# Optimization experiments

Hardware: AMD Instinct MI355X
Metric: run time of the kernel (lower is better)

The kernel has to match this reference:

```python
import jax, jax.numpy as jnp
import numpy as np


def setup_inputs() -> dict:
    key = jax.random.key(0)
    k1, k2, k3, k4 = jax.random.split(key, 4)
    B, A, C = 16, 65536, 21  # batch, anchors, num_classes+1 (20 fg classes + background)
    loc_preds = jax.random.normal(k1, (B, A, 4), dtype=jnp.float32)
    loc_targets = jax.random.normal(k2, (B, A, 4), dtype=jnp.float32)
    cls_preds = jax.random.normal(k3, (B, A, C), dtype=jnp.float32)
    # -1 = ignore, 0 = background/negative, 1..20 = positive classes
    cls_targets = jax.random.randint(k4, (B, A), -1, C)
    pos = cls_targets > 0
    return {
        "loc_preds": loc_preds,
        "loc_targets": loc_targets,
        "cls_preds": cls_preds,
        "cls_targets": cls_targets,
        "pos": pos,
        "verbose": 0,
    }


def reference(loc_preds, loc_targets, cls_preds, cls_targets, pos, verbose):
    eps = 1e-7
    num_pos = jnp.sum(pos).astype(loc_preds.dtype)

    # smooth L1 over positive anchors (sum reduction, beta=1), mask instead of gather
    posf = pos[..., None].astype(loc_preds.dtype)          # [B, A, 1]
    d = loc_preds - loc_targets
    ad = jnp.abs(d)
    sl1 = jnp.where(ad < 1.0, 0.5 * d * d, ad - 0.5)
    loc_loss = jnp.sum(sl1 * posf)

    # focal loss over non-ignored anchors (cls_targets > -1)
    pos_neg = (cls_targets > -1)[..., None].astype(cls_preds.dtype)  # [B, A, 1]
    C = cls_preds.shape[-1]
    y = jax.nn.one_hot(cls_targets, C, dtype=cls_preds.dtype)  # -1 -> all zeros
    p = jax.nn.softmax(cls_preds, axis=-1)
    p = jnp.clip(p, eps, 1.0 - eps)
    fl = -y * jnp.log(p) * (1.0 - p) ** 2
    cls_loss = jnp.sum(fl * pos_neg)

    return (loc_loss + cls_loss) / num_pos
```

## Files before the change

### kernel.cpp

```cpp
#include <hip/hip_runtime.h>

#define NCLS 21
#define BLK 256
#define CHUNK 256
#define STAGE_BYTES (CHUNK * NCLS * 4)

__device__ __forceinline__ void load_lds16(const void* g, void* l) {
    __builtin_amdgcn_global_load_lds(
        (const __attribute__((address_space(1))) unsigned int*)g,
        (__attribute__((address_space(3))) unsigned int*)l,
        16, 0, 0);
}

__global__ __launch_bounds__(BLK) void focal_main(
    const float* __restrict__ loc_p,
    const float* __restrict__ loc_t,
    const float* __restrict__ cls_p,
    const int*   __restrict__ cls_t,
    float2* __restrict__ partials,
    int n_anchors)
{
    __shared__ float lds[CHUNK * NCLS];
    __shared__ float red[8];

    const int tid  = threadIdx.x;
    const int wave = tid >> 6;
    const int lane = tid & 63;
    const long long anchor0 = (long long)blockIdx.x * CHUNK;
    const long long a = anchor0 + tid;

    if (anchor0 + CHUNK <= n_anchors) {
        const char* gbase = (const char*)(cls_p + anchor0 * NCLS);
        char* lbase = (char*)lds;
        #pragma unroll
        for (int k = wave; k < NCLS; k += 4) {
            load_lds16(gbase + k * 1024 + lane * 16, lbase + k * 1024);
        }
    } else {
        long long rem = n_anchors - anchor0;
        int valid = rem > 0 ? (int)(rem * NCLS) : 0;
        for (int i = tid; i < valid; i += BLK)
            lds[i] = cls_p[anchor0 * NCLS + i];
    }

    int t = -1;
    float4 lp = make_float4(0.f, 0.f, 0.f, 0.f);
    float4 lt = make_float4(0.f, 0.f, 0.f, 0.f);
    if (a < n_anchors) {
        t  = cls_t[a];
        lp = ((const float4*)loc_p)[a];
        lt = ((const float4*)loc_t)[a];
    }

    float acc  = 0.0f;
    float npos = 0.0f;
    {
        float d0 = lp.x - lt.x, d1 = lp.y - lt.y, d2 = lp.z - lt.z, d3 = lp.w - lt.w;
        float a0 = fabsf(d0), a1 = fabsf(d1), a2 = fabsf(d2), a3 = fabsf(d3);
        float s = 0.0f;
        s += (a0 < 1.0f) ? 0.5f * d0 * d0 : a0 - 0.5f;
        s += (a1 < 1.0f) ? 0.5f * d1 * d1 : a1 - 0.5f;
        s += (a2 < 1.0f) ? 0.5f * d2 * d2 : a2 - 0.5f;
        s += (a3 < 1.0f) ? 0.5f * d3 * d3 : a3 - 0.5f;
        if (t > 0) { acc = s; npos = 1.0f; }
    }

    __syncthreads();

    if (t >= 0) {
        const float* row = lds + tid * NCLS;
        float m = row[0];
        #pragma unroll
        for (int j = 1; j < NCLS; ++j) m = fmaxf(m, row[j]);
        float s = 0.0f;
        #pragma unroll
        for (int j = 0; j < NCLS; ++j) s += __expf(row[j] - m);
        float pt = __expf(row[t] - m) / s;
        pt = fminf(fmaxf(pt, 1e-7f), 1.0f - 1e-7f);
        float om = 1.0f - pt;
        acc += -__logf(pt) * om * om;
    }

    #pragma unroll
    for (int off = 32; off > 0; off >>= 1) {
        acc  += __shfl_down(acc,  off, 64);
        npos += __shfl_down(npos, off, 64);
    }
    if (lane == 0) { red[wave * 2] = acc; red[wave * 2 + 1] = npos; }
    __syncthreads();
    if (tid == 0) {
        float L = red[0] + red[2] + red[4] + red[6];
        float P = red[1] + red[3] + red[5] + red[7];
        partials[blockIdx.x] = make_float2(L, P);
    }
}

__global__ __launch_bounds__(BLK) void focal_reduce(
    const float2* __restrict__ partials, float* __restrict__ out, int npart)
{
    __shared__ float red[8];
    float L = 0.0f, P = 0.0f;
    for (int i = threadIdx.x; i < npart; i += BLK) {
        float2 v = partials[i];
        L += v.x; P += v.y;
    }
    #pragma unroll
    for (int off = 32; off > 0; off >>= 1) {
        L += __shfl_down(L, off, 64);
        P += __shfl_down(P, off, 64);
    }
    const int wave = threadIdx.x >> 6, lane = threadIdx.x & 63;
    if (lane == 0) { red[wave * 2] = L; red[wave * 2 + 1] = P; }
    __syncthreads();
    if (threadIdx.x == 0) {
        float Ls = red[0] + red[2] + red[4] + red[6];
        float Ps = red[1] + red[3] + red[5] + red[7];
        out[0] = Ls / Ps;
    }
}

extern "C" void kernel_launch(void* const* d_in, const int* in_sizes, int n_in,
                              void* d_out, int out_size, void* d_ws, size_t ws_size,
                              hipStream_t stream)
{
    const float* loc_p = (const float*)d_in[0];
    const float* loc_t = (const float*)d_in[1];
    const float* cls_p = (const float*)d_in[2];
    const int*   cls_t = (const int*)d_in[3];
    float*  out = (float*)d_out;
    float2* ws  = (float2*)d_ws;

    const int n_anchors = in_sizes[3];
    const int blocks = (n_anchors + CHUNK - 1) / CHUNK;

    focal_main<<<blocks, BLK, 0, stream>>>(loc_p, loc_t, cls_p, cls_t, ws, n_anchors);
    focal_reduce<<<1, BLK, 0, stream>>>(ws, out, blocks);
}
```

Measured before the change: 169.2 us.

## Make LDS staging per-wave and drop block barriers in focal loss kernel

```diff
diff --git a/kernel.cpp b/kernel.cpp
--- a/kernel.cpp
+++ b/kernel.cpp
@@ -3,13 +3,28 @@
 #define NCLS 21
 #define BLK 256
 #define CHUNK 256
-#define STAGE_BYTES (CHUNK * NCLS * 4)
+#define WAVE_ANCHORS 64
+#define WAVE_BYTES (WAVE_ANCHORS * NCLS * 4)
+#define WAITCNT_VM0 0x0F70
 
 __device__ __forceinline__ void load_lds16(const void* g, void* l) {
     __builtin_amdgcn_global_load_lds(
         (const __attribute__((address_space(1))) unsigned int*)g,
         (__attribute__((address_space(3))) unsigned int*)l,
         16, 0, 0);
+}
+
+__device__ __forceinline__ float focal_row(const float* __restrict__ row, int t) {
+    float m = row[0];
+    #pragma unroll
+    for (int j = 1; j < NCLS; ++j) m = fmaxf(m, row[j]);
+    float s = 0.0f;
+    #pragma unroll
+    for (int j = 0; j < NCLS; ++j) s += __expf(row[j] - m);
+    float pt = __expf(row[t] - m) / s;
+    pt = fminf(fmaxf(pt, 1e-7f), 1.0f - 1e-7f);
+    float om = 1.0f - pt;
+    return -__logf(pt) * om * om;
 }
 
 __global__ __launch_bounds__(BLK) void focal_main(
@@ -20,27 +35,23 @@
     float2* __restrict__ partials,
     int n_anchors)
 {
-    __shared__ float lds[CHUNK * NCLS];
-    __shared__ float red[8];
+    __shared__ float lds[CHUNK * NCLS + 192];
 
     const int tid  = threadIdx.x;
     const int wave = tid >> 6;
     const int lane = tid & 63;
     const long long anchor0 = (long long)blockIdx.x * CHUNK;
     const long long a = anchor0 + tid;
+    const bool full = (anchor0 + CHUNK <= n_anchors);
 
-    if (anchor0 + CHUNK <= n_anchors) {
-        const char* gbase = (const char*)(cls_p + anchor0 * NCLS);
-        char* lbase = (char*)lds;
+    if (full) {
+        const char* gw = (const char*)(cls_p + (anchor0 + (long long)wave * WAVE_ANCHORS) * NCLS);
+        char* lw = (char*)lds + wave * WAVE_BYTES;
         #pragma unroll
-        for (int k = wave; k < NCLS; k += 4) {
-            load_lds16(gbase + k * 1024 + lane * 16, lbase + k * 1024);
-        }
-    } else {
-        long long rem = n_anchors - anchor0;
-        int valid = rem > 0 ? (int)(rem * NCLS) : 0;
-        for (int i = tid; i < valid; i += BLK)
-            lds[i] = cls_p[anchor0 * NCLS + i];
+        for (int k = 0; k < 5; ++k)
+            load_lds16(gw + k * 1024 + lane * 16, lw + k * 1024);
+        if (lane < 16)
+            load_lds16(gw + 5120 + lane * 16, lw + 5120);
     }
 
     int t = -1;
@@ -65,20 +76,12 @@
         if (t > 0) { acc = s; npos = 1.0f; }
     }
 
-    __syncthreads();
-
-    if (t >= 0) {
-        const float* row = lds + tid * NCLS;
-        float m = row[0];
-        #pragma unroll
-        for (int j = 1; j < NCLS; ++j) m = fmaxf(m, row[j]);
-        float s = 0.0f;
-        #pragma unroll
-        for (int j = 0; j < NCLS; ++j) s += __expf(row[j] - m);
-        float pt = __expf(row[t] - m) / s;
-        pt = fminf(fmaxf(pt, 1e-7f), 1.0f - 1e-7f);
-        float om = 1.0f - pt;
-        acc += -__logf(pt) * om * om;
+    if (full) {
+        __builtin_amdgcn_s_waitcnt(WAITCNT_VM0);
+        if (t >= 0)
+            acc += focal_row(lds + tid * NCLS, t);
+    } else if (t >= 0) {
+        acc += focal_row(cls_p + a * NCLS, t);
     }
 
     #pragma unroll
@@ -86,21 +89,17 @@
         acc  += __shfl_down(acc,  off, 64);
         npos += __shfl_down(npos, off, 64);
     }
-    if (lane == 0) { red[wave * 2] = acc; red[wave * 2 + 1] = npos; }
-    __syncthreads();
-    if (tid == 0) {
-        float L = red[0] + red[2] + red[4] + red[6];
-        float P = red[1] + red[3] + red[5] + red[7];
-        partials[blockIdx.x] = make_float2(L, P);
-    }
+    if (lane == 0)
+        partials[blockIdx.x * 4 + wave] = make_float2(acc, npos);
 }
 
-__global__ __launch_bounds__(BLK) void focal_reduce(
+#define RBLK 1024
+__global__ __launch_bounds__(RBLK) void focal_reduce(
     const float2* __restrict__ partials, float* __restrict__ out, int npart)
 {
-    __shared__ float red[8];
+    __shared__ float red[32];
     float L = 0.0f, P = 0.0f;
-    for (int i = threadIdx.x; i < npart; i += BLK) {
+    for (int i = threadIdx.x; i < npart; i += RBLK) {
         float2 v = partials[i];
         L += v.x; P += v.y;
     }
@@ -113,8 +112,9 @@
     if (lane == 0) { red[wave * 2] = L; red[wave * 2 + 1] = P; }
     __syncthreads();
     if (threadIdx.x == 0) {
-        float Ls = red[0] + red[2] + red[4] + red[6];
-        float Ps = red[1] + red[3] + red[5] + red[7];
+        float Ls = 0.0f, Ps = 0.0f;
+        #pragma unroll
+        for (int w = 0; w < RBLK / 64; ++w) { Ls += red[w * 2]; Ps += red[w * 2 + 1]; }
         out[0] = Ls / Ps;
     }
 }
@@ -134,5 +134,5 @@
     const int blocks = (n_anchors + CHUNK - 1) / CHUNK;
 
     focal_main<<<blocks, BLK, 0, stream>>>(loc_p, loc_t, cls_p, cls_t, ws, n_anchors);
-    focal_reduce<<<1, BLK, 0, stream>>>(ws, out, blocks);
+    focal_reduce<<<1, RBLK, 0, stream>>>(ws, out, blocks * 4);
 }
```

Measured after the change: 168.6 us. About the same (-0.3%).
